# Kernel optimization log

Measured on AMD Instinct MI355X. Metric: run time of the kernel, lower is better.

Reference implementation:

```python
import jax, jax.numpy as jnp
import numpy as np

W_DENSITY, W_COUNT, W_DOMAIN, W_REGIONAL = 100.0, 0.001, 0.5, 1.0
LEVELS = (1, 2, 3)


def setup_inputs() -> dict:
    key = jax.random.key(0)
    k1, k2, k3, k4 = jax.random.split(key, 4)
    B, H, W = 32, 768, 768
    return {
        "pred_density": jax.random.uniform(k1, (B, 1, H, W), dtype=jnp.float32),
        "gt_density": jax.random.uniform(k2, (B, 1, H, W), dtype=jnp.float32),
        "domain_pred_rgb": jax.random.normal(k3, (B, 2), dtype=jnp.float32),
        "domain_pred_thermal": jax.random.normal(k4, (B, 2), dtype=jnp.float32),
    }


def _regional_loss(pred, gt):
    # pred, gt: [B, 1, H, W]; H, W divisible by 2**max(LEVELS)
    B, C, H, W = pred.shape
    total = jnp.float32(0.0)
    last_cells = 1
    for L in LEVELS:
        cells = 2 ** L
        hs, ws = H // cells, W // cells
        # region sums via reshape: [B, C, cells, cells]
        p = pred.reshape(B, C, cells, hs, cells, ws).sum(axis=(3, 5))
        g = gt.reshape(B, C, cells, hs, cells, ws).sum(axis=(3, 5))
        # per-region L1 loss = mean over (B, C), summed over the cells x cells grid
        total = total + jnp.abs(p - g).mean(axis=(0, 1)).sum()
        last_cells = cells
    return total / (len(LEVELS) * last_cells * last_cells)


def _ce_loss(logits, labels):
    # mean over batch of -log_softmax(logits)[label]
    logp = jax.nn.log_softmax(logits, axis=-1)
    return -jnp.take_along_axis(logp, labels[:, None], axis=-1).mean()


def reference(pred_density, gt_density, domain_pred_rgb, domain_pred_thermal):
    B = pred_density.shape[0]
    density_loss = jnp.mean((pred_density - gt_density) ** 2)
    pred_count = pred_density.sum(axis=(2, 3)).squeeze()  # [B]
    gt_count = gt_density.sum(axis=(2, 3)).squeeze()
    count_loss = jnp.abs(pred_count - gt_count).mean()
    regional = _regional_loss(pred_density, gt_density)
    rgb_labels = jnp.zeros((B,), dtype=jnp.int32)
    thermal_labels = jnp.ones((B,), dtype=jnp.int32)
    domain_loss = (_ce_loss(domain_pred_rgb, rgb_labels)
                   + _ce_loss(domain_pred_thermal, thermal_labels)) / 2.0
    total_loss = (W_DENSITY * density_loss + W_COUNT * count_loss
                  + W_REGIONAL * regional + W_DOMAIN * domain_loss)
    return total_loss
```

## Files before the change

kernel.cpp:

```cpp
#include <hip/hip_runtime.h>
#include <math.h>

#define BATCH 32
#define HH 768
#define WW 768
#define NREG 64
#define NBLK (BATCH * NREG)

__global__ __launch_bounds__(256) void region_reduce(
    const float* __restrict__ pred, const float* __restrict__ gt,
    float* __restrict__ sq_out, float* __restrict__ dws)
{
    const int bid   = blockIdx.x;
    const int b     = bid >> 6;
    const int ri    = (bid >> 3) & 7;
    const int chunk = bid & 7;
    const size_t base = (size_t)b * (HH * WW) + (size_t)(ri * 96 + chunk * 12) * WW;

    const int t = threadIdx.x;
    const int g = t >> 5;
    const int l = t & 31;

    const float* __restrict__ pb = pred + base + g * 96;
    const float* __restrict__ gb = gt   + base + g * 96;

    int offs[9];
    #pragma unroll
    for (int k = 0; k < 9; ++k) {
        const int q   = l + 32 * k;
        const int row = q / 24;
        const int c   = q - row * 24;
        offs[k] = row * WW + c * 4;
    }
    float4 p[9], q4[9];
    #pragma unroll
    for (int k = 0; k < 9; ++k) p[k]  = *(const float4*)(pb + offs[k]);
    #pragma unroll
    for (int k = 0; k < 9; ++k) q4[k] = *(const float4*)(gb + offs[k]);

    float sq = 0.f, ds = 0.f;
    #pragma unroll
    for (int k = 0; k < 9; ++k) {
        const float dx = p[k].x - q4[k].x;
        const float dy = p[k].y - q4[k].y;
        const float dz = p[k].z - q4[k].z;
        const float dw = p[k].w - q4[k].w;
        sq += (dx * dx + dy * dy) + (dz * dz + dw * dw);
        ds += (dx + dy) + (dz + dw);
    }

    #pragma unroll
    for (int off = 16; off > 0; off >>= 1) ds += __shfl_down(ds, off, 64);
    #pragma unroll
    for (int off = 32; off > 0; off >>= 1) sq += __shfl_down(sq, off, 64);

    if (l == 0) dws[((((b << 3) + ri) << 3) + g) * 8 + chunk] = ds;

    __shared__ float lsq[4];
    const int wave = t >> 6;
    if ((t & 63) == 0) lsq[wave] = sq;
    __syncthreads();
    if (t == 0) sq_out[bid] = (lsq[0] + lsq[1]) + (lsq[2] + lsq[3]);
}

__global__ __launch_bounds__(256) void finalize(
    const float* __restrict__ sq, const float* __restrict__ dws,
    const float* __restrict__ rgb, const float* __restrict__ th,
    float* __restrict__ out)
{
    __shared__ float d[NBLK];
    __shared__ float d2[BATCH * 16];
    __shared__ float d1[BATCH * 4];
    __shared__ float redbuf[4 * 6];
    const int t = threadIdx.x;

    float s_sq = 0.f;
    const float4* sq4 = (const float4*)sq;
    #pragma unroll
    for (int k = 0; k < 2; ++k) {
        const float4 v = sq4[t + 256 * k];
        s_sq += (v.x + v.y) + (v.z + v.w);
    }

    float l3 = 0.f;
    #pragma unroll
    for (int k = 0; k < 8; ++k) {
        const int r = t + 256 * k;
        const float4* dp = (const float4*)(dws + r * 8);
        const float4 a = dp[0], bb = dp[1];
        const float v = ((a.x + a.y) + (a.z + a.w)) + ((bb.x + bb.y) + (bb.z + bb.w));
        d[r] = v;
        l3 += fabsf(v);
    }
    __syncthreads();

    float l2 = 0.f;
    #pragma unroll
    for (int k = 0; k < 2; ++k) {
        const int i = t + 256 * k;
        const int b = i >> 4, r2 = i & 15;
        const int i2 = r2 >> 2, j2 = r2 & 3;
        const float* db = d + b * 64;
        const float v = (db[(2 * i2) * 8 + 2 * j2]     + db[(2 * i2) * 8 + 2 * j2 + 1])
                      + (db[(2 * i2 + 1) * 8 + 2 * j2] + db[(2 * i2 + 1) * 8 + 2 * j2 + 1]);
        d2[i] = v;
        l2 += fabsf(v);
    }
    __syncthreads();

    float l1 = 0.f;
    if (t < BATCH * 4) {
        const int b = t >> 2, r1 = t & 3;
        const int i1 = r1 >> 1, j1 = r1 & 1;
        const float* db = d2 + b * 16;
        const float v = (db[(2 * i1) * 4 + 2 * j1]     + db[(2 * i1) * 4 + 2 * j1 + 1])
                      + (db[(2 * i1 + 1) * 4 + 2 * j1] + db[(2 * i1 + 1) * 4 + 2 * j1 + 1]);
        d1[t] = v;
        l1 = fabsf(v);
    }
    __syncthreads();

    float cnt = 0.f, dom = 0.f;
    if (t < BATCH) {
        const float c = (d1[t * 4] + d1[t * 4 + 1]) + (d1[t * 4 + 2] + d1[t * 4 + 3]);
        cnt = fabsf(c);
        const float x0 = rgb[t * 2], x1 = rgb[t * 2 + 1];
        const float mx = fmaxf(x0, x1);
        dom  = (mx + logf(expf(x0 - mx) + expf(x1 - mx))) - x0;
        const float y0 = th[t * 2], y1 = th[t * 2 + 1];
        const float my = fmaxf(y0, y1);
        dom += (my + logf(expf(y0 - my) + expf(y1 - my))) - y1;
    }

    float vals[6] = {s_sq, l3, l2, l1, cnt, dom};
    #pragma unroll
    for (int off = 32; off > 0; off >>= 1) {
        #pragma unroll
        for (int j = 0; j < 6; ++j) vals[j] += __shfl_down(vals[j], off, 64);
    }
    const int wave = t >> 6;
    if ((t & 63) == 0) {
        #pragma unroll
        for (int j = 0; j < 6; ++j) redbuf[wave * 6 + j] = vals[j];
    }
    __syncthreads();
    if (t == 0) {
        float S[6];
        #pragma unroll
        for (int j = 0; j < 6; ++j)
            S[j] = (redbuf[j] + redbuf[6 + j]) + (redbuf[12 + j] + redbuf[18 + j]);
        const float density  = S[0] / (float)((size_t)BATCH * HH * WW);
        const float count_l  = S[4] / (float)BATCH;
        const float regional = ((S[3] + S[2] + S[1]) / (float)BATCH) / 192.0f;
        const float domain   = S[5] / 64.0f;
        out[0] = 100.0f * density + 0.001f * count_l + 1.0f * regional + 0.5f * domain;
    }
}

extern "C" void kernel_launch(void* const* d_in, const int* in_sizes, int n_in,
                              void* d_out, int out_size, void* d_ws, size_t ws_size,
                              hipStream_t stream) {
    const float* pred = (const float*)d_in[0];
    const float* gt   = (const float*)d_in[1];
    const float* rgb  = (const float*)d_in[2];
    const float* th   = (const float*)d_in[3];
    float* out = (float*)d_out;

    float* sq  = (float*)d_ws;
    float* dws = sq + NBLK;

    region_reduce<<<NBLK, 256, 0, stream>>>(pred, gt, sq, dws);
    finalize<<<1, 256, 0, stream>>>(sq, dws, rgb, th, out);
}
```

Measured before the change: 171.7 us.

## Halve block count and software-pipeline loads with inline asm double buffering

Each block now covers 24 rows instead of 12, so the grid drops from 2048 to 1024 blocks. Loads are issued as inline-asm global_load_dwordx4 into two register buffers, with explicit s_waitcnt so the next batch is in flight while the current one is consumed. This targets memory latency and per-block overhead in a bandwidth-bound reduction. In exchange it uses more VGPRs and relies on hand-written vmcnt accounting that the compiler cannot check; finalize is adjusted to the new partial-sum layout.

```diff
diff --git a/kernel.cpp b/kernel.cpp
--- a/kernel.cpp
+++ b/kernel.cpp
@@ -4,57 +4,92 @@
 #define BATCH 32
 #define HH 768
 #define WW 768
-#define NREG 64
-#define NBLK (BATCH * NREG)
+
+typedef float v4f __attribute__((ext_vector_type(4)));
 
 __global__ __launch_bounds__(256) void region_reduce(
     const float* __restrict__ pred, const float* __restrict__ gt,
     float* __restrict__ sq_out, float* __restrict__ dws)
 {
-    const int bid   = blockIdx.x;
-    const int b     = bid >> 6;
-    const int ri    = (bid >> 3) & 7;
-    const int chunk = bid & 7;
-    const size_t base = (size_t)b * (HH * WW) + (size_t)(ri * 96 + chunk * 12) * WW;
+    const int bid = blockIdx.x;
+    const int b   = bid >> 5;
+    const int ri  = (bid >> 2) & 7;
+    const int qt  = bid & 3;
+    const size_t base = (size_t)b * (HH * WW) + (size_t)(ri * 96 + qt * 24) * WW;
 
     const int t = threadIdx.x;
     const int g = t >> 5;
     const int l = t & 31;
 
-    const float* __restrict__ pb = pred + base + g * 96;
-    const float* __restrict__ gb = gt   + base + g * 96;
-
-    int offs[9];
-    #pragma unroll
-    for (int k = 0; k < 9; ++k) {
-        const int q   = l + 32 * k;
+    const float* pb = pred + base;
+    const float* gb = gt   + base;
+
+    unsigned off0[6];
+    #pragma unroll
+    for (int k = 0; k < 6; ++k) {
+        const int q = l + 32 * k;
         const int row = q / 24;
         const int c   = q - row * 24;
-        offs[k] = row * WW + c * 4;
-    }
-    float4 p[9], q4[9];
-    #pragma unroll
-    for (int k = 0; k < 9; ++k) p[k]  = *(const float4*)(pb + offs[k]);
-    #pragma unroll
-    for (int k = 0; k < 9; ++k) q4[k] = *(const float4*)(gb + offs[k]);
-
+        off0[k] = (unsigned)((row * WW + g * 96 + c * 4) * sizeof(float));
+    }
+
+    v4f P[2][6], G[2][6];
     float sq = 0.f, ds = 0.f;
-    #pragma unroll
-    for (int k = 0; k < 9; ++k) {
-        const float dx = p[k].x - q4[k].x;
-        const float dy = p[k].y - q4[k].y;
-        const float dz = p[k].z - q4[k].z;
-        const float dw = p[k].w - q4[k].w;
-        sq += (dx * dx + dy * dy) + (dz * dz + dw * dw);
-        ds += (dx + dy) + (dz + dw);
-    }
-
-    #pragma unroll
-    for (int off = 16; off > 0; off >>= 1) ds += __shfl_down(ds, off, 64);
-    #pragma unroll
-    for (int off = 32; off > 0; off >>= 1) sq += __shfl_down(sq, off, 64);
-
-    if (l == 0) dws[((((b << 3) + ri) << 3) + g) * 8 + chunk] = ds;
+
+#define ISSUE(S, DISP)                                                        \
+    {                                                                         \
+        _Pragma("unroll") for (int k = 0; k < 6; ++k) {                       \
+            asm volatile("global_load_dwordx4 %0, %1, %2"                     \
+                         : "=&v"(P[S][k]) : "v"(off0[k] + (DISP)), "s"(pb));  \
+        }                                                                     \
+        _Pragma("unroll") for (int k = 0; k < 6; ++k) {                       \
+            asm volatile("global_load_dwordx4 %0, %1, %2"                     \
+                         : "=&v"(G[S][k]) : "v"(off0[k] + (DISP)), "s"(gb));  \
+        }                                                                     \
+    }
+
+#define WAITN(S, N)                                                           \
+    asm volatile("s_waitcnt vmcnt(" #N ")"                                    \
+                 : "+v"(P[S][0]), "+v"(P[S][1]), "+v"(P[S][2]),               \
+                   "+v"(P[S][3]), "+v"(P[S][4]), "+v"(P[S][5]),               \
+                   "+v"(G[S][0]), "+v"(G[S][1]), "+v"(G[S][2]),               \
+                   "+v"(G[S][3]), "+v"(G[S][4]), "+v"(G[S][5]) :: "memory");
+
+#define CONSUME(S)                                                            \
+    {                                                                         \
+        _Pragma("unroll") for (int k = 0; k < 6; ++k) {                       \
+            const float dx = P[S][k][0] - G[S][k][0];                         \
+            const float dy = P[S][k][1] - G[S][k][1];                         \
+            const float dz = P[S][k][2] - G[S][k][2];                         \
+            const float dw = P[S][k][3] - G[S][k][3];                         \
+            sq += (dx * dx + dy * dy) + (dz * dz + dw * dw);                  \
+            ds += (dx + dy) + (dz + dw);                                      \
+        }                                                                     \
+    }
+
+    ISSUE(0, 0u)
+    ISSUE(1, 24576u)
+    WAITN(0, 12)
+    CONSUME(0)
+    ISSUE(0, 49152u)
+    WAITN(1, 12)
+    CONSUME(1)
+    WAITN(0, 0)
+    CONSUME(0)
+
+#undef ISSUE
+#undef WAITN
+#undef CONSUME
+
+    #pragma unroll
+    for (int o = 16; o > 0; o >>= 1) ds += __shfl_down(ds, o, 64);
+    #pragma unroll
+    for (int o = 32; o > 0; o >>= 1) sq += __shfl_down(sq, o, 64);
+
+    if (l == 0) {
+        const int r = ((b << 3) + ri) * 8 + g;
+        dws[r * 4 + qt] = ds;
+    }
 
     __shared__ float lsq[4];
     const int wave = t >> 6;
@@ -68,27 +103,24 @@
     const float* __restrict__ rgb, const float* __restrict__ th,
     float* __restrict__ out)
 {
-    __shared__ float d[NBLK];
+    __shared__ float d[2048];
     __shared__ float d2[BATCH * 16];
     __shared__ float d1[BATCH * 4];
     __shared__ float redbuf[4 * 6];
     const int t = threadIdx.x;
 
     float s_sq = 0.f;
-    const float4* sq4 = (const float4*)sq;
-    #pragma unroll
-    for (int k = 0; k < 2; ++k) {
-        const float4 v = sq4[t + 256 * k];
-        s_sq += (v.x + v.y) + (v.z + v.w);
+    {
+        const float4 v = ((const float4*)sq)[t];
+        s_sq = (v.x + v.y) + (v.z + v.w);
     }
 
     float l3 = 0.f;
     #pragma unroll
     for (int k = 0; k < 8; ++k) {
         const int r = t + 256 * k;
-        const float4* dp = (const float4*)(dws + r * 8);
-        const float4 a = dp[0], bb = dp[1];
-        const float v = ((a.x + a.y) + (a.z + a.w)) + ((bb.x + bb.y) + (bb.z + bb.w));
+        const float4 a = ((const float4*)dws)[r];
+        const float v = (a.x + a.y) + (a.z + a.w);
         d[r] = v;
         l3 += fabsf(v);
     }
@@ -167,8 +199,8 @@
     float* out = (float*)d_out;
 
     float* sq  = (float*)d_ws;
-    float* dws = sq + NBLK;
-
-    region_reduce<<<NBLK, 256, 0, stream>>>(pred, gt, sq, dws);
+    float* dws = sq + 1024;
+
+    region_reduce<<<1024, 256, 0, stream>>>(pred, gt, sq, dws);
     finalize<<<1, 256, 0, stream>>>(sq, dws, rgb, th, out);
 }
```

After: 171.6 us. No clear change (-0.1%).

## Fuse region reduce and finalize into one kernel with last-block atomic completion

Applied to the files above, without the earlier changes.

Merges the two kernels into one: blocks accumulate per-region diff sums and squared-error partials into zeroed workspace with atomics, and the last block to finish, found through an atomic counter, runs the hierarchical finalize. Global loads become nontemporal and are interleaved with the arithmetic instead of all being issued up front. This removes a second kernel launch and the intermediate workspace round trip, but adds a memset launch, atomic contention on 64 squared-error slots, and thread fences.

```diff
diff --git a/kernel.cpp b/kernel.cpp
--- a/kernel.cpp
+++ b/kernel.cpp
@@ -4,13 +4,20 @@
 #define BATCH 32
 #define HH 768
 #define WW 768
-#define NREG 64
-#define NBLK (BATCH * NREG)
+#define NBLK 2048
 
-__global__ __launch_bounds__(256) void region_reduce(
+typedef float v4f __attribute__((ext_vector_type(4)));
+
+
+__global__ __launch_bounds__(256) void fused_loss(
     const float* __restrict__ pred, const float* __restrict__ gt,
-    float* __restrict__ sq_out, float* __restrict__ dws)
+    const float* __restrict__ rgb, const float* __restrict__ th,
+    float* __restrict__ out, float* __restrict__ ws)
 {
+    float* sqb = ws;
+    unsigned* ctr = (unsigned*)(ws + 64);
+    float* dreg = ws + 128;
+
     const int bid   = blockIdx.x;
     const int b     = bid >> 6;
     const int ri    = (bid >> 3) & 7;
@@ -21,76 +28,54 @@
     const int g = t >> 5;
     const int l = t & 31;
 
-    const float* __restrict__ pb = pred + base + g * 96;
-    const float* __restrict__ gb = gt   + base + g * 96;
+    const float* pb = pred + base + g * 96;
+    const float* gb = gt   + base + g * 96;
 
-    int offs[9];
+    float sq = 0.f, ds = 0.f;
     #pragma unroll
     for (int k = 0; k < 9; ++k) {
         const int q   = l + 32 * k;
         const int row = q / 24;
         const int c   = q - row * 24;
-        offs[k] = row * WW + c * 4;
-    }
-    float4 p[9], q4[9];
-    #pragma unroll
-    for (int k = 0; k < 9; ++k) p[k]  = *(const float4*)(pb + offs[k]);
-    #pragma unroll
-    for (int k = 0; k < 9; ++k) q4[k] = *(const float4*)(gb + offs[k]);
-
-    float sq = 0.f, ds = 0.f;
-    #pragma unroll
-    for (int k = 0; k < 9; ++k) {
-        const float dx = p[k].x - q4[k].x;
-        const float dy = p[k].y - q4[k].y;
-        const float dz = p[k].z - q4[k].z;
-        const float dw = p[k].w - q4[k].w;
+        const v4f p  = __builtin_nontemporal_load((const v4f*)(pb + row * WW + c * 4));
+        const v4f gg = __builtin_nontemporal_load((const v4f*)(gb + row * WW + c * 4));
+        const float dx = p[0] - gg[0], dy = p[1] - gg[1];
+        const float dz = p[2] - gg[2], dw = p[3] - gg[3];
         sq += (dx * dx + dy * dy) + (dz * dz + dw * dw);
         ds += (dx + dy) + (dz + dw);
     }
 
     #pragma unroll
-    for (int off = 16; off > 0; off >>= 1) ds += __shfl_down(ds, off, 64);
+    for (int o = 16; o > 0; o >>= 1) ds += __shfl_down(ds, o, 64);
     #pragma unroll
-    for (int off = 32; off > 0; off >>= 1) sq += __shfl_down(sq, off, 64);
+    for (int o = 32; o > 0; o >>= 1) sq += __shfl_down(sq, o, 64);
 
-    if (l == 0) dws[((((b << 3) + ri) << 3) + g) * 8 + chunk] = ds;
+    if (l == 0)        atomicAdd(&dreg[((b << 3) + ri) * 8 + g], ds);
+    if ((t & 63) == 0) atomicAdd(&sqb[bid & 63], sq);
 
-    __shared__ float lsq[4];
-    const int wave = t >> 6;
-    if ((t & 63) == 0) lsq[wave] = sq;
+    __threadfence();
     __syncthreads();
-    if (t == 0) sq_out[bid] = (lsq[0] + lsq[1]) + (lsq[2] + lsq[3]);
-}
+    __shared__ unsigned s_last;
+    if (t == 0) s_last = (atomicAdd(ctr, 1u) == (unsigned)(NBLK - 1)) ? 1u : 0u;
+    __syncthreads();
+    if (s_last == 0) return;
+    __threadfence();
 
-__global__ __launch_bounds__(256) void finalize(
-    const float* __restrict__ sq, const float* __restrict__ dws,
-    const float* __restrict__ rgb, const float* __restrict__ th,
-    float* __restrict__ out)
-{
-    __shared__ float d[NBLK];
+    __shared__ float d[2048];
     __shared__ float d2[BATCH * 16];
     __shared__ float d1[BATCH * 4];
     __shared__ float redbuf[4 * 6];
-    const int t = threadIdx.x;
 
-    float s_sq = 0.f;
-    const float4* sq4 = (const float4*)sq;
-    #pragma unroll
-    for (int k = 0; k < 2; ++k) {
-        const float4 v = sq4[t + 256 * k];
-        s_sq += (v.x + v.y) + (v.z + v.w);
-    }
+    float s_sq = (t < 64) ? sqb[t] : 0.f;
 
     float l3 = 0.f;
     #pragma unroll
-    for (int k = 0; k < 8; ++k) {
-        const int r = t + 256 * k;
-        const float4* dp = (const float4*)(dws + r * 8);
-        const float4 a = dp[0], bb = dp[1];
-        const float v = ((a.x + a.y) + (a.z + a.w)) + ((bb.x + bb.y) + (bb.z + bb.w));
-        d[r] = v;
-        l3 += fabsf(v);
+    for (int k = 0; k < 2; ++k) {
+        const int i4 = t + 256 * k;
+        const v4f v = ((const v4f*)dreg)[i4];
+        d[4 * i4 + 0] = v[0]; d[4 * i4 + 1] = v[1];
+        d[4 * i4 + 2] = v[2]; d[4 * i4 + 3] = v[3];
+        l3 += (fabsf(v[0]) + fabsf(v[1])) + (fabsf(v[2]) + fabsf(v[3]));
     }
     __syncthreads();
 
@@ -98,9 +83,9 @@
     #pragma unroll
     for (int k = 0; k < 2; ++k) {
         const int i = t + 256 * k;
-        const int b = i >> 4, r2 = i & 15;
+        const int bb = i >> 4, r2 = i & 15;
         const int i2 = r2 >> 2, j2 = r2 & 3;
-        const float* db = d + b * 64;
+        const float* db = d + bb * 64;
         const float v = (db[(2 * i2) * 8 + 2 * j2]     + db[(2 * i2) * 8 + 2 * j2 + 1])
                       + (db[(2 * i2 + 1) * 8 + 2 * j2] + db[(2 * i2 + 1) * 8 + 2 * j2 + 1]);
         d2[i] = v;
@@ -110,9 +95,9 @@
 
     float l1 = 0.f;
     if (t < BATCH * 4) {
-        const int b = t >> 2, r1 = t & 3;
+        const int bb = t >> 2, r1 = t & 3;
         const int i1 = r1 >> 1, j1 = r1 & 1;
-        const float* db = d2 + b * 16;
+        const float* db = d2 + bb * 16;
         const float v = (db[(2 * i1) * 4 + 2 * j1]     + db[(2 * i1) * 4 + 2 * j1 + 1])
                       + (db[(2 * i1 + 1) * 4 + 2 * j1] + db[(2 * i1 + 1) * 4 + 2 * j1 + 1]);
         d1[t] = v;
@@ -165,10 +150,8 @@
     const float* rgb  = (const float*)d_in[2];
     const float* th   = (const float*)d_in[3];
     float* out = (float*)d_out;
+    float* ws  = (float*)d_ws;
 
-    float* sq  = (float*)d_ws;
-    float* dws = sq + NBLK;
-
-    region_reduce<<<NBLK, 256, 0, stream>>>(pred, gt, sq, dws);
-    finalize<<<1, 256, 0, stream>>>(sq, dws, rgb, th, out);
+    (void)hipMemsetAsync(d_ws, 0, 8704, stream);
+    fused_loss<<<NBLK, 256, 0, stream>>>(pred, gt, rgb, th, out, ws);
 }
```

Measured after the change: 499.1 us. +190.7%, slower.
